# Performance work log

Measured on AMD Instinct MI355X. Metric: run time of the kernel, lower is better.

## Reference

```python
import jax, jax.numpy as jnp
import numpy as np

D_MODEL = 512
N_HEADS = 8
UPDATE_STEPS = 2


def setup_inputs() -> dict:
    key = jax.random.key(0)
    k1, k2 = jax.random.split(key)
    B, L, S = 2, 2048, 2048
    R = jax.random.normal(k1, (B, L, D_MODEL), dtype=jnp.float32)
    Y = jax.random.normal(k2, (B, S, D_MODEL), dtype=jnp.float32)
    return {"R": R, "Y": Y}


def reference(R, Y):
    B, L, _ = R.shape
    _, S, _ = Y.shape
    H = N_HEADS
    E = D_MODEL // H  # head dim
    scale = 1.0 / jnp.sqrt(jnp.asarray(E, dtype=R.dtype))

    q = R.reshape(B, L, H, E)
    k = Y.reshape(B, S, H, E)
    v = k  # keys == values == stored patterns

    # Iterative Hopfield update: queries replaced by attention readout each step.
    for _ in range(UPDATE_STEPS):
        scores = jnp.einsum('blhe,bshe->bhls', q, k)  # [B,H,L,S]
        A = jax.nn.softmax(scale * scores, axis=-1)
        q = jnp.einsum('bhls,bshd->blhd', A, v)  # [B,L,H,E]

    return q.reshape(B, L, H * E)
```

## Files before the change

### kernel.cpp

```cpp
#include <hip/hip_runtime.h>
#include <hip/hip_bf16.h>
#include <cstdint>


typedef __attribute__((ext_vector_type(8))) short bf16x8;
typedef __attribute__((ext_vector_type(4))) short short4v;
typedef __attribute__((ext_vector_type(4))) float f32x4;

constexpr int B_ = 2, L_ = 2048, S_ = 2048, H_ = 8, E_ = 64, DM_ = 512;
constexpr int NTQ_ = 16;
constexpr float SCALE2 = 0.18033688011112042f;
constexpr float FIXMAX = 24.0f;

__device__ __forceinline__ ushort f2bf(float a) {
  uint32_t u = __builtin_bit_cast(uint32_t, a);
  return (ushort)((u + 0x7fffu + ((u >> 16) & 1u)) >> 16);
}
__device__ __forceinline__ uint32_t pk2(float a, float b) {
  ushort u0 = __builtin_bit_cast(ushort, __float2bfloat16(a));
  ushort u1 = __builtin_bit_cast(ushort, __float2bfloat16(b));
  return (uint32_t)u0 | ((uint32_t)u1 << 16);
}
__device__ __forceinline__ void dma16(const ushort* g, const ushort* l) {
  __builtin_amdgcn_global_load_lds(
      (const __attribute__((address_space(1))) uint32_t*)g,
      (__attribute__((address_space(3))) uint32_t*)l, 16, 0, 0);
}

__global__ void cvt_kernel(const float* __restrict__ in, ushort* __restrict__ out, int n4) {
  int i = blockIdx.x * 256 + threadIdx.x;
  if (i >= n4) return;
  float4 v = reinterpret_cast<const float4*>(in)[i];
  ushort4 o;
  o.x = f2bf(v.x); o.y = f2bf(v.y); o.z = f2bf(v.z); o.w = f2bf(v.w);
  reinterpret_cast<ushort4*>(out)[i] = o;
}

__global__ __launch_bounds__(256, 4) void hopfield_kernel(
    const float* __restrict__ Rf, const ushort* __restrict__ Yb,
    float* __restrict__ outF) {
  __shared__ ushort Vq[4][2][2048];
  __shared__ uint32_t SB[1024];

  const int tid = threadIdx.x, lane = tid & 63, wid = tid >> 6;
  const int g = lane >> 4, qi = lane & 15;
  const int wg = blockIdx.x, qt = wg & 63, h = (wg >> 6) & 7, b = wg >> 9;

  size_t qbase[2];
#pragma unroll
  for (int set = 0; set < 2; ++set)
    qbase[set] = (size_t)(b * L_ + qt * 32 + set * 16 + qi) * DM_ + h * E_;

  bf16x8 qf[2][2];
#pragma unroll
  for (int set = 0; set < 2; ++set)
#pragma unroll
    for (int eck = 0; eck < 2; ++eck) {
      const float* s = Rf + qbase[set] + eck * 32 + 8 * g;
      float4 aa = *reinterpret_cast<const float4*>(s);
      float4 bb = *reinterpret_cast<const float4*>(s + 4);
      uint4 w;
      w.x = pk2(aa.x * SCALE2, aa.y * SCALE2);
      w.y = pk2(aa.z * SCALE2, aa.w * SCALE2);
      w.z = pk2(bb.x * SCALE2, bb.y * SCALE2);
      w.w = pk2(bb.z * SCALE2, bb.w * SCALE2);
      qf[set][eck] = __builtin_bit_cast(bf16x8, w);
    }

  const size_t ybase = (size_t)(b * S_ + wid * 512) * DM_ + h * E_;

  const ushort* gdma[4];
#pragma unroll
  for (int i = 0; i < 4; ++i) {
    int c = i * 64 + lane, blk = c >> 3;
    int s = (blk & 3) * 8 + ((blk >> 4) & 1) * 4 + ((c >> 1) & 3);
    int e0 = ((blk >> 2) & 3) * 16 + (c & 1) * 8;
    gdma[i] = Yb + ybase + (size_t)s * DM_ + e0;
  }

  int kidx[4];
#pragma unroll
  for (int nt = 0; nt < 2; ++nt)
#pragma unroll
    for (int eck = 0; eck < 2; ++eck) {
      int s = nt * 16 + qi;
      kidx[nt * 2 + eck] = ((((s >> 2) & 1) * 4 + (eck * 2 + (g >> 1))) * 4 + (s >> 3)) * 64 +
                           (s & 3) * 16 + 8 * (g & 1);
    }

  const uint32_t vb0 = (uint32_t)(uintptr_t)(&Vq[wid][0][0]);
  float* mrg = (float*)&Vq[0][0][0];
  float* ml = (float*)&SB[0];
  ushort* qls = (ushort*)&SB[0];

  for (int pass = 0; pass < 2; ++pass) {
    f32x4 oacc[2][4];
#pragma unroll
    for (int set = 0; set < 2; ++set)
#pragma unroll
      for (int et = 0; et < 4; ++et) oacc[set][et] = f32x4{0.f, 0.f, 0.f, 0.f};
    float ls[2] = {0.f, 0.f};

#pragma unroll
    for (int i = 0; i < 4; ++i) dma16(gdma[i], &Vq[wid][0][i * 512]);
    int cur = 0;

    for (int t = 0; t < NTQ_; ++t) {
      asm volatile("s_waitcnt vmcnt(0)" ::: "memory");
      if (t + 1 < NTQ_) {
        const size_t tadd = (size_t)(t + 1) * 32 * DM_;
#pragma unroll
        for (int i = 0; i < 4; ++i)
          dma16(gdma[i] + tadd, &Vq[wid][cur ^ 1][i * 512]);
      }

      const ushort* Vc = &Vq[wid][cur][0];
      const uint32_t trbase = vb0 + (uint32_t)(cur * 4096) + 8u * (uint32_t)lane;

      bf16x8 kf[4];
#pragma unroll
      for (int i = 0; i < 4; ++i)
        kf[i] = *reinterpret_cast<const bf16x8*>(&Vc[kidx[i]]);

      bf16x8 pfrag[2];
#pragma unroll
      for (int set = 0; set < 2; ++set) {
        f32x4 st[2];
        __builtin_amdgcn_s_setprio(1);
#pragma unroll
        for (int nt = 0; nt < 2; ++nt) {
          f32x4 acc = f32x4{-FIXMAX, -FIXMAX, -FIXMAX, -FIXMAX};
          acc = __builtin_amdgcn_mfma_f32_16x16x32_bf16(kf[nt * 2 + 0], qf[set][0], acc, 0, 0, 0);
          acc = __builtin_amdgcn_mfma_f32_16x16x32_bf16(kf[nt * 2 + 1], qf[set][1], acc, 0, 0, 0);
          st[nt] = acc;
        }
        __builtin_amdgcn_s_setprio(0);
        float p0 = __builtin_amdgcn_exp2f(st[0][0]);
        float p1 = __builtin_amdgcn_exp2f(st[0][1]);
        float p2 = __builtin_amdgcn_exp2f(st[0][2]);
        float p3 = __builtin_amdgcn_exp2f(st[0][3]);
        float p4 = __builtin_amdgcn_exp2f(st[1][0]);
        float p5 = __builtin_amdgcn_exp2f(st[1][1]);
        float p6 = __builtin_amdgcn_exp2f(st[1][2]);
        float p7 = __builtin_amdgcn_exp2f(st[1][3]);
        ls[set] += ((p0 + p1) + (p2 + p3)) + ((p4 + p5) + (p6 + p7));
        uint32_t a0 = pk2(p0, p1), b0 = pk2(p2, p3);
        uint32_t a1 = pk2(p4, p5), b1 = pk2(p6, p7);
        asm("v_permlane32_swap_b32 %0, %1" : "+v"(a0), "+v"(a1));
        asm("v_permlane16_swap_b32 %0, %1" : "+v"(a0), "+v"(a1));
        asm("v_permlane32_swap_b32 %0, %1" : "+v"(b0), "+v"(b1));
        asm("v_permlane16_swap_b32 %0, %1" : "+v"(b0), "+v"(b1));
        uint4 pw;
        pw.x = a0; pw.y = b0; pw.z = a1; pw.w = b1;
        pfrag[set] = __builtin_bit_cast(bf16x8, pw);
      }

      {
        short4v tr[4][2];
#pragma unroll
        for (int et = 0; et < 4; ++et) {
          asm volatile("ds_read_b64_tr_b16 %0, %1 offset:%2"
                       : "=v"(tr[et][0]) : "v"(trbase), "i"(et * 512));
          asm volatile("ds_read_b64_tr_b16 %0, %1 offset:%2"
                       : "=v"(tr[et][1]) : "v"(trbase), "i"((4 + et) * 512));
        }
        asm volatile("s_waitcnt lgkmcnt(0)" ::: "memory");
        __builtin_amdgcn_sched_barrier(0);

        __builtin_amdgcn_s_setprio(1);
#pragma unroll
        for (int et = 0; et < 4; ++et) {
          short4v lo = tr[et][0], hi = tr[et][1];
          bf16x8 vf;
          vf[0] = lo[0]; vf[1] = lo[1]; vf[2] = lo[2]; vf[3] = lo[3];
          vf[4] = hi[0]; vf[5] = hi[1]; vf[6] = hi[2]; vf[7] = hi[3];
#pragma unroll
          for (int set = 0; set < 2; ++set)
            oacc[set][et] = __builtin_amdgcn_mfma_f32_16x16x32_bf16(vf, pfrag[set], oacc[set][et], 0, 0, 0);
        }
        __builtin_amdgcn_s_setprio(0);
      }
      cur ^= 1;
    }

#pragma unroll
    for (int set = 0; set < 2; ++set) {
      ls[set] += __shfl_xor(ls[set], 16);
      ls[set] += __shfl_xor(ls[set], 32);
    }

#pragma unroll
    for (int set = 0; set < 2; ++set) {
#pragma unroll
      for (int et = 0; et < 4; ++et)
        *reinterpret_cast<f32x4*>(&mrg[(((wid * 2 + set) * 4 + et) * 64 + lane) * 4]) =
            oacc[set][et];
      ml[(wid * 2 + set) * 64 + lane] = ls[set];
    }
    __syncthreads();

    if (pass == 0) {
      uint2 qw[2];
#pragma unroll
      for (int set = 0; set < 2; ++set) {
        float lt = 0.f;
#pragma unroll
        for (int w = 0; w < 4; ++w) lt += ml[(w * 2 + set) * 64 + lane];
        float fac = SCALE2 / lt;
        f32x4 Ot = f32x4{0.f, 0.f, 0.f, 0.f};
#pragma unroll
        for (int w = 0; w < 4; ++w)
          Ot += *reinterpret_cast<const f32x4*>(&mrg[(((w * 2 + set) * 4 + wid) * 64 + lane) * 4]);
        qw[set].x = pk2(Ot[0] * fac, Ot[1] * fac);
        qw[set].y = pk2(Ot[2] * fac, Ot[3] * fac);
      }
      __syncthreads();
#pragma unroll
      for (int set = 0; set < 2; ++set)
        *reinterpret_cast<uint2*>(&qls[(set * 16 + qi) * 64 + wid * 16 + 4 * g]) = qw[set];
      __syncthreads();
#pragma unroll
      for (int set = 0; set < 2; ++set)
#pragma unroll
        for (int eck = 0; eck < 2; ++eck)
          qf[set][eck] = *reinterpret_cast<const bf16x8*>(
              &qls[(set * 16 + qi) * 64 + eck * 32 + 8 * g]);
      __syncthreads();
    } else {
      if (wid == 0) {
#pragma unroll
        for (int set = 0; set < 2; ++set) {
          float lt = 0.f;
#pragma unroll
          for (int w = 0; w < 4; ++w) lt += ml[(w * 2 + set) * 64 + lane];
          float inv = 1.0f / lt;
#pragma unroll
          for (int et = 0; et < 4; ++et) {
            f32x4 Ot = f32x4{0.f, 0.f, 0.f, 0.f};
#pragma unroll
            for (int w = 0; w < 4; ++w)
              Ot += *reinterpret_cast<const f32x4*>(&mrg[(((w * 2 + set) * 4 + et) * 64 + lane) * 4]);
            float4 o;
            o.x = Ot[0] * inv; o.y = Ot[1] * inv; o.z = Ot[2] * inv; o.w = Ot[3] * inv;
            *reinterpret_cast<float4*>(&outF[qbase[set] + et * 16 + 4 * g]) = o;
          }
        }
      }
    }
  }
}

extern "C" void kernel_launch(void* const* d_in, const int* in_sizes, int n_in,
                              void* d_out, int out_size, void* d_ws, size_t ws_size,
                              hipStream_t stream) {
  const float* R = (const float*)d_in[0];
  const float* Y = (const float*)d_in[1];
  float* outF = (float*)d_out;

  constexpr int NE = B_ * S_ * DM_;
  ushort* Yb = (ushort*)d_ws;

  const int n4 = NE / 4;
  cvt_kernel<<<dim3((n4 + 255) / 256), 256, 0, stream>>>(Y, Yb, n4);

  const int ngrid = B_ * H_ * (L_ / 32);
  hopfield_kernel<<<dim3(ngrid), 256, 0, stream>>>(R, Yb, outF);
}
```

Baseline: 63.04 us.

## Compute softmax row sums via ones-MFMA, use packed bf16 cvt, remap blocks

Drops the per-lane VALU summation of exponentials and its cross-lane shuffle reduction. The row sums are now accumulated with an extra MFMA against a ones fragment, so the sum uses the same bf16-rounded probabilities as the PV product. Replaces the software bf16 packing with the hardware v_cvt_pk_bf16_f32 instruction. Also remaps block indices so consecutive blocks land on different heads/batches, presumably to spread work across XCDs or improve cache locality. The cost is two extra MFMAs per tile, in exchange for fewer VALU ops in the softmax path.

```diff
diff --git a/kernel.cpp b/kernel.cpp
--- a/kernel.cpp
+++ b/kernel.cpp
@@ -16,10 +16,10 @@
   uint32_t u = __builtin_bit_cast(uint32_t, a);
   return (ushort)((u + 0x7fffu + ((u >> 16) & 1u)) >> 16);
 }
-__device__ __forceinline__ uint32_t pk2(float a, float b) {
-  ushort u0 = __builtin_bit_cast(ushort, __float2bfloat16(a));
-  ushort u1 = __builtin_bit_cast(ushort, __float2bfloat16(b));
-  return (uint32_t)u0 | ((uint32_t)u1 << 16);
+__device__ __forceinline__ uint32_t pkcvt(float lo, float hi) {
+  uint32_t r;
+  asm("v_cvt_pk_bf16_f32 %0, %1, %2" : "=v"(r) : "v"(lo), "v"(hi));
+  return r;
 }
 __device__ __forceinline__ void dma16(const ushort* g, const ushort* l) {
   __builtin_amdgcn_global_load_lds(
@@ -44,7 +44,8 @@
 
   const int tid = threadIdx.x, lane = tid & 63, wid = tid >> 6;
   const int g = lane >> 4, qi = lane & 15;
-  const int wg = blockIdx.x, qt = wg & 63, h = (wg >> 6) & 7, b = wg >> 9;
+  const int wg = (blockIdx.x & 7) * 128 + (blockIdx.x >> 3);
+  const int qt = wg & 63, h = (wg >> 6) & 7, b = wg >> 9;
 
   size_t qbase[2];
 #pragma unroll
@@ -60,10 +61,10 @@
       float4 aa = *reinterpret_cast<const float4*>(s);
       float4 bb = *reinterpret_cast<const float4*>(s + 4);
       uint4 w;
-      w.x = pk2(aa.x * SCALE2, aa.y * SCALE2);
-      w.y = pk2(aa.z * SCALE2, aa.w * SCALE2);
-      w.z = pk2(bb.x * SCALE2, bb.y * SCALE2);
-      w.w = pk2(bb.z * SCALE2, bb.w * SCALE2);
+      w.x = pkcvt(aa.x * SCALE2, aa.y * SCALE2);
+      w.y = pkcvt(aa.z * SCALE2, aa.w * SCALE2);
+      w.z = pkcvt(bb.x * SCALE2, bb.y * SCALE2);
+      w.w = pkcvt(bb.z * SCALE2, bb.w * SCALE2);
       qf[set][eck] = __builtin_bit_cast(bf16x8, w);
     }
 
@@ -88,18 +89,23 @@
                            (s & 3) * 16 + 8 * (g & 1);
     }
 
+  uint4 ou;
+  ou.x = ou.y = ou.z = ou.w = 0x3F803F80u;
+  const bf16x8 ones = __builtin_bit_cast(bf16x8, ou);
+
   const uint32_t vb0 = (uint32_t)(uintptr_t)(&Vq[wid][0][0]);
   float* mrg = (float*)&Vq[0][0][0];
   float* ml = (float*)&SB[0];
   ushort* qls = (ushort*)&SB[0];
 
   for (int pass = 0; pass < 2; ++pass) {
-    f32x4 oacc[2][4];
-#pragma unroll
-    for (int set = 0; set < 2; ++set)
+    f32x4 oacc[2][4], lacc[2];
+#pragma unroll
+    for (int set = 0; set < 2; ++set) {
 #pragma unroll
       for (int et = 0; et < 4; ++et) oacc[set][et] = f32x4{0.f, 0.f, 0.f, 0.f};
-    float ls[2] = {0.f, 0.f};
+      lacc[set] = f32x4{0.f, 0.f, 0.f, 0.f};
+    }
 
 #pragma unroll
     for (int i = 0; i < 4; ++i) dma16(gdma[i], &Vq[wid][0][i * 512]);
@@ -143,9 +149,8 @@
         float p5 = __builtin_amdgcn_exp2f(st[1][1]);
         float p6 = __builtin_amdgcn_exp2f(st[1][2]);
         float p7 = __builtin_amdgcn_exp2f(st[1][3]);
-        ls[set] += ((p0 + p1) + (p2 + p3)) + ((p4 + p5) + (p6 + p7));
-        uint32_t a0 = pk2(p0, p1), b0 = pk2(p2, p3);
-        uint32_t a1 = pk2(p4, p5), b1 = pk2(p6, p7);
+        uint32_t a0 = pkcvt(p0, p1), b0 = pkcvt(p2, p3);
+        uint32_t a1 = pkcvt(p4, p5), b1 = pkcvt(p6, p7);
         asm("v_permlane32_swap_b32 %0, %1" : "+v"(a0), "+v"(a1));
         asm("v_permlane16_swap_b32 %0, %1" : "+v"(a0), "+v"(a1));
         asm("v_permlane32_swap_b32 %0, %1" : "+v"(b0), "+v"(b1));
@@ -169,6 +174,9 @@
 
         __builtin_amdgcn_s_setprio(1);
 #pragma unroll
+        for (int set = 0; set < 2; ++set)
+          lacc[set] = __builtin_amdgcn_mfma_f32_16x16x32_bf16(ones, pfrag[set], lacc[set], 0, 0, 0);
+#pragma unroll
         for (int et = 0; et < 4; ++et) {
           short4v lo = tr[et][0], hi = tr[et][1];
           bf16x8 vf;
@@ -185,17 +193,11 @@
 
 #pragma unroll
     for (int set = 0; set < 2; ++set) {
-      ls[set] += __shfl_xor(ls[set], 16);
-      ls[set] += __shfl_xor(ls[set], 32);
-    }
-
-#pragma unroll
-    for (int set = 0; set < 2; ++set) {
 #pragma unroll
       for (int et = 0; et < 4; ++et)
         *reinterpret_cast<f32x4*>(&mrg[(((wid * 2 + set) * 4 + et) * 64 + lane) * 4]) =
             oacc[set][et];
-      ml[(wid * 2 + set) * 64 + lane] = ls[set];
+      ml[(wid * 2 + set) * 64 + lane] = lacc[set][0];
     }
     __syncthreads();
 
@@ -211,8 +213,8 @@
 #pragma unroll
         for (int w = 0; w < 4; ++w)
           Ot += *reinterpret_cast<const f32x4*>(&mrg[(((w * 2 + set) * 4 + wid) * 64 + lane) * 4]);
-        qw[set].x = pk2(Ot[0] * fac, Ot[1] * fac);
-        qw[set].y = pk2(Ot[2] * fac, Ot[3] * fac);
+        qw[set].x = pkcvt(Ot[0] * fac, Ot[1] * fac);
+        qw[set].y = pkcvt(Ot[2] * fac, Ot[3] * fac);
       }
       __syncthreads();
 #pragma unroll
```

Result: faster. 55.72 us (-11.6%).
